# Kernel tuning notes

Hardware: AMD Instinct MI355X
Metric: run time of the kernel (lower is better)

The kernel has to match this reference:

```python
import jax, jax.numpy as jnp
import numpy as np

N = 100000      # nodes
E = 1600000     # edges (avg degree 16)
D = 128         # in_feats
C = 40          # n_classes
K = 4           # propagation steps
T = 2.0
DELTA = T / K   # 0.5
EPS = 1e-5      # LayerNorm eps


def setup_inputs() -> dict:
    key = jax.random.key(0)
    k1, k2, k3, k4, k5 = jax.random.split(key, 5)
    feat = jax.random.normal(k1, (N, D), jnp.float32)
    row = jax.random.randint(k2, (E,), 0, N, dtype=jnp.int32)
    col = jax.random.randint(k3, (E,), 0, N, dtype=jnp.int32)
    # fc: Linear(D -> C), xavier-ish scale
    W = jax.random.normal(k4, (C, D), jnp.float32) / np.sqrt(D)
    b = jax.random.normal(k5, (C,), jnp.float32) * 0.01
    # LayerNorm params
    gamma = jnp.ones((C,), jnp.float32)
    beta = jnp.zeros((C,), jnp.float32)
    return {"feat": feat, "row": row, "col": col, "W": W, "b": b,
            "gamma": gamma, "beta": beta}


def reference(feat, row, col, W, b, gamma, beta):
    # degrees of augmented adjacency A + I (row counts + self loop)
    deg = jnp.zeros((N,), feat.dtype).at[row].add(1.0) + 1.0
    dinv = jax.lax.rsqrt(deg)
    w_edge = dinv[row] * dinv[col]     # S[row,col] for off-diagonal entries
    w_self = dinv * dinv               # S[i,i] from the added self loop
    # h <- ((1-delta) I + delta S)^K @ feat, applied iteratively (same math as
    # precomputing the matrix power, but never materializes it)
    h = feat
    for _ in range(K):
        agg = jax.ops.segment_sum(h[col] * w_edge[:, None], row, num_segments=N)
        agg = agg + h * w_self[:, None]
        h = (1.0 - DELTA) * h + DELTA * agg
    # fc
    h = h @ W.T + b                    # [N, C]
    # LayerNorm over last dim
    mu = jnp.mean(h, axis=-1, keepdims=True)
    var = jnp.var(h, axis=-1, keepdims=True)
    h = (h - mu) * jax.lax.rsqrt(var + EPS) * gamma + beta
    return h
```

## Files before the change

### kernel.cpp

```cpp
#include <hip/hip_runtime.h>
#include <hip/hip_fp16.h>

#define N_NODES 100000
#define N_EDGES 1600000
#define D_FEAT  128
#define C_CLS   40
#define ZSTRIDE 32
#define LN_EPS  1e-5f

#define RPB   256
#define NBKT  ((N_NODES + RPB - 1) / RPB)
#define BCAP  6144
#define TILE_E 4096
#define EBLK  ((N_EDGES + TILE_E - 1) / TILE_E)
#define NTILES (N_NODES / 16)
#define FCB   ((NTILES + 3) / 4)

typedef __attribute__((ext_vector_type(8))) _Float16 half8;
typedef __attribute__((ext_vector_type(4))) float floatx4;
typedef __attribute__((ext_vector_type(2))) int   intx2;
typedef __attribute__((ext_vector_type(4))) unsigned uintx4;

__device__ inline float2 h2f2(unsigned v) {
    __half2 h = *(__half2*)&v;
    return __half22float2(h);
}
__device__ inline unsigned f2h2(float x, float y) {
    __half2 h = __floats2half2_rn(x, y);
    return *(unsigned*)&h;
}

__global__ __launch_bounds__(256) void fcbin_k(const float* __restrict__ feat,
                                               const float* __restrict__ W,
                                               const int* __restrict__ row,
                                               const int* __restrict__ col,
                                               int* __restrict__ bktsz,
                                               int* __restrict__ csr_tmp,
                                               unsigned* __restrict__ z) {
    __shared__ int hist[NBKT];
    __shared__ int cbase[NBKT];
    __shared__ _Float16 zl[4][16][64];
    int t = threadIdx.x;
    if (blockIdx.x < EBLK) {
        int tile = blockIdx.x * TILE_E;
        for (int i = t; i < NBKT; i += 256) hist[i] = 0;
        __syncthreads();
        int r[16], c[16], pos[16];
        #pragma unroll
        for (int k = 0; k < 16; k++) {
            int e = tile + k * 256 + t;
            if (e < N_EDGES) {
                r[k] = row[e]; c[k] = col[e];
                pos[k] = atomicAdd(&hist[r[k] / RPB], 1);
            } else r[k] = -1;
        }
        __syncthreads();
        for (int i = t; i < NBKT; i += 256) {
            int h = hist[i];
            cbase[i] = h ? atomicAdd(&bktsz[i], h) : 0;
        }
        __syncthreads();
        #pragma unroll
        for (int k = 0; k < 16; k++) {
            if (r[k] >= 0) {
                int b = r[k] / RPB;
                int slot = cbase[b] + pos[k];
                if (slot < BCAP)
                    csr_tmp[b * BCAP + slot] = ((r[k] & (RPB - 1)) << 17) | c[k];
            }
        }
        return;
    }
    int wave = t >> 6, lane = t & 63;
    int m = lane & 15, quad = lane >> 4;
    int tile = (blockIdx.x - EBLK) * 4 + wave;
    bool valid = (tile < NTILES);
    int node0 = tile * 16;

    half8 bfrag[3][4];
    if (valid) {
        #pragma unroll
        for (int ct = 0; ct < 3; ct++) {
            int c = ct * 16 + m;
            bool ok = (c < C_CLS);
            #pragma unroll
            for (int ks = 0; ks < 4; ks++) {
                const float* wr = W + c * D_FEAT + ks * 32 + quad * 8;
                #pragma unroll
                for (int j = 0; j < 8; j++)
                    bfrag[ct][ks][j] = ok ? (_Float16)wr[j] : (_Float16)0.0f;
            }
        }
    }

    floatx4 acc0 = {0.f,0.f,0.f,0.f}, acc1 = acc0, acc2 = acc0;
    if (valid) {
        #pragma unroll
        for (int ks = 0; ks < 4; ks++) {
            const float4* ap = (const float4*)&feat[(node0 + m) * D_FEAT + ks * 32 + quad * 8];
            float4 a0 = ap[0], a1 = ap[1];
            half8 afrag;
            afrag[0] = (_Float16)a0.x; afrag[1] = (_Float16)a0.y;
            afrag[2] = (_Float16)a0.z; afrag[3] = (_Float16)a0.w;
            afrag[4] = (_Float16)a1.x; afrag[5] = (_Float16)a1.y;
            afrag[6] = (_Float16)a1.z; afrag[7] = (_Float16)a1.w;
            acc0 = __builtin_amdgcn_mfma_f32_16x16x32_f16(afrag, bfrag[0][ks], acc0, 0, 0, 0);
            acc1 = __builtin_amdgcn_mfma_f32_16x16x32_f16(afrag, bfrag[1][ks], acc1, 0, 0, 0);
            acc2 = __builtin_amdgcn_mfma_f32_16x16x32_f16(afrag, bfrag[2][ks], acc2, 0, 0, 0);
        }
    }

    {
        int zr = lane >> 2;
        uint2 zz = make_uint2(0u, 0u);
        ((uint2*)&zl[wave][zr][48])[lane & 3] = zz;
    }
    if (valid) {
        #pragma unroll
        for (int r = 0; r < 4; r++) {
            int zrow = quad * 4 + r;
            zl[wave][zrow][m]      = (_Float16)acc0[r];
            zl[wave][zrow][16 + m] = (_Float16)acc1[r];
            zl[wave][zrow][32 + m] = (_Float16)acc2[r];
        }
    }
    __syncthreads();
    if (valid) {
        int zr = lane >> 2, part = lane & 3;
        uint4 v0 = ((uint4*)&zl[wave][zr][0])[part];
        uint4 v1 = ((uint4*)&zl[wave][zr][0])[part + 4];
        uint4* zg = (uint4*)z;
        zg[(size_t)(node0 + zr) * 8 + part]     = v0;
        zg[(size_t)(node0 + zr) * 8 + part + 4] = v1;
    }
}

__global__ __launch_bounds__(256) void refineA_k(const int* __restrict__ csr_tmp,
                                                 const int* __restrict__ bktsz,
                                                 int2* __restrict__ rowinfo,
                                                 float* __restrict__ dinv,
                                                 float* __restrict__ selfc) {
    __shared__ int hist[RPB];
    __shared__ int psc[RPB];
    int b = blockIdx.x, t = threadIdx.x;
    int r0 = b * RPB;
    int nrows = min(RPB, N_NODES - r0);
    hist[t] = 0;
    __syncthreads();
    int cnt = bktsz[b];
    const int* base = csr_tmp + b * BCAP;
    for (int i = t; i < cnt; i += 256)
        atomicAdd(&hist[base[i] >> 17], 1);
    __syncthreads();
    int v = hist[t];
    psc[t] = v;
    __syncthreads();
    for (int off = 1; off < 256; off <<= 1) {
        int x = (t >= off) ? psc[t - off] : 0;
        __syncthreads();
        psc[t] += x;
        __syncthreads();
    }
    if (t < nrows) {
        int start = b * BCAP + psc[t] - v;
        float d = rsqrtf((float)v + 1.0f);
        rowinfo[r0 + t] = make_int2(start, start + v);
        dinv[r0 + t]  = d;
        selfc[r0 + t] = 0.5f + 0.5f * d * d;
    }
}

__global__ __launch_bounds__(256) void refineB_k(const int* __restrict__ csr_tmp,
                                                 const int* __restrict__ bktsz,
                                                 const int2* __restrict__ rowinfo,
                                                 const float* __restrict__ dinv,
                                                 int2* __restrict__ csr) {
    __shared__ int   cur[RPB];
    __shared__ float dl[RPB];
    int b = blockIdx.x, t = threadIdx.x;
    int r0 = b * RPB;
    int nrows = min(RPB, N_NODES - r0);
    if (t < nrows) {
        cur[t] = rowinfo[r0 + t].x;
        dl[t]  = dinv[r0 + t];
    }
    __syncthreads();
    int cnt = bktsz[b];
    const int* base = csr_tmp + b * BCAP;
    for (int i = t; i < cnt; i += 256) {
        int pk = base[i];
        int lr = pk >> 17;
        int c  = pk & 0x1FFFF;
        int p = atomicAdd(&cur[lr], 1);
        float w = (0.5f * dl[lr]) * dinv[c];
        csr[p] = make_int2(c, __float_as_int(w));
    }
}

__global__ __launch_bounds__(256) void prop_z_k(const unsigned* __restrict__ hin,
                                                unsigned* __restrict__ hout,
                                                const int2* __restrict__ rowinfo,
                                                const int2* __restrict__ csr,
                                                const float* __restrict__ selfc) {
    int t = threadIdx.x;
    int wave = t >> 6, lane = t & 63;
    int q   = lane >> 3;
    int sub = lane & 7;
    int node = blockIdx.x * 32 + wave * 8 + q;
    const uintx4* hin4 = (const uintx4*)hin;

    uintx4 hv = hin4[(unsigned)node * 8 + sub];
    float sc = selfc[node];
    float acc[8];
    {
        float2 f0 = h2f2(hv.x), f1 = h2f2(hv.y), f2 = h2f2(hv.z), f3 = h2f2(hv.w);
        acc[0] = f0.x * sc; acc[1] = f0.y * sc;
        acc[2] = f1.x * sc; acc[3] = f1.y * sc;
        acc[4] = f2.x * sc; acc[5] = f2.y * sc;
        acc[6] = f3.x * sc; acc[7] = f3.y * sc;
    }

    int2 ri = rowinfo[node];
    int j = ri.x, end = ri.y;
    int base = ri.x;

    int2 e[8];
    #pragma unroll
    for (int k = 0; k < 8; k++) {
        int idx = (j + k < end) ? j + k : base;
        e[k] = csr[idx];
    }

    while (__any(j < end)) {
        uintx4 g[8];
        float w[8];
        #pragma unroll
        for (int k = 0; k < 8; k++) {
            bool val = (j + k < end);
            int  c   = val ? e[k].x : 0;
            w[k]     = val ? __int_as_float(e[k].y) : 0.0f;
            g[k] = hin4[(unsigned)c * 8 + sub];
        }
        int j2 = j + 8;
        #pragma unroll
        for (int k = 0; k < 8; k++) {
            int idx = (j2 + k < end) ? j2 + k : base;
            e[k] = csr[idx];
        }
        #pragma unroll
        for (int k = 0; k < 8; k++) {
            float2 f0 = h2f2(g[k].x), f1 = h2f2(g[k].y), f2 = h2f2(g[k].z), f3 = h2f2(g[k].w);
            acc[0] += w[k] * f0.x; acc[1] += w[k] * f0.y;
            acc[2] += w[k] * f1.x; acc[3] += w[k] * f1.y;
            acc[4] += w[k] * f2.x; acc[5] += w[k] * f2.y;
            acc[6] += w[k] * f3.x; acc[7] += w[k] * f3.y;
        }
        j = j2;
    }

    uintx4 o;
    o.x = f2h2(acc[0], acc[1]);
    o.y = f2h2(acc[2], acc[3]);
    o.z = f2h2(acc[4], acc[5]);
    o.w = f2h2(acc[6], acc[7]);
    ((uintx4*)hout)[(unsigned)node * 8 + sub] = o;
}

__global__ __launch_bounds__(256) void ln_k(const unsigned* __restrict__ z,
                                            const float* __restrict__ b,
                                            const float* __restrict__ gamma,
                                            const float* __restrict__ beta,
                                            float* __restrict__ out) {
    int t = threadIdx.x;
    int node = blockIdx.x * 64 + (t >> 2);
    int p = t & 2 ? (t & 3) : (t & 3);
    p = t & 3;
    if (node >= N_NODES) return;

    float v[16];
    float s = 0.0f, ss = 0.0f;
    int cb = p * 16;
    int nreal = (p < 2) ? 16 : (p == 2 ? 8 : 0);
    if (nreal) {
        const uint4* zr = (const uint4*)z + (size_t)node * 8;
        uint4 a0 = zr[p * 2], a1 = zr[p * 2 + 1];
        unsigned u[8] = {a0.x, a0.y, a0.z, a0.w, a1.x, a1.y, a1.z, a1.w};
        #pragma unroll
        for (int i = 0; i < 8; i++) {
            float2 f = h2f2(u[i]);
            v[2 * i] = f.x; v[2 * i + 1] = f.y;
        }
        for (int i = 0; i < nreal; i++) {
            v[i] += b[cb + i];
            s += v[i];
            ss += v[i] * v[i];
        }
    }
    s  += __shfl_xor(s, 1);  s  += __shfl_xor(s, 2);
    ss += __shfl_xor(ss, 1); ss += __shfl_xor(ss, 2);

    float mean = s * (1.0f / C_CLS);
    float var  = ss * (1.0f / C_CLS) - mean * mean;
    float inv  = rsqrtf(var + LN_EPS);
    if (nreal) {
        float* orow = out + (size_t)node * C_CLS + cb;
        for (int i = 0; i < nreal; i++)
            orow[i] = (v[i] - mean) * inv * gamma[cb + i] + beta[cb + i];
    }
}

extern "C" void kernel_launch(void* const* d_in, const int* in_sizes, int n_in,
                              void* d_out, int out_size, void* d_ws, size_t ws_size,
                              hipStream_t stream) {
    const float* feat  = (const float*)d_in[0];
    const int*   row   = (const int*)d_in[1];
    const int*   col   = (const int*)d_in[2];
    const float* W     = (const float*)d_in[3];
    const float* b     = (const float*)d_in[4];
    const float* gamma = (const float*)d_in[5];
    const float* beta  = (const float*)d_in[6];
    float* out = (float*)d_out;

    char* ws = (char*)d_ws;
    size_t off = 0;
    auto alloc = [&](size_t bytes) {
        size_t o = off;
        off = (off + bytes + 255) & ~(size_t)255;
        return o;
    };
    float*    dinv     = (float*)   (ws + alloc((size_t)N_NODES * 4));
    float*    selfc    = (float*)   (ws + alloc((size_t)N_NODES * 4));
    int2*     rowinfo  = (int2*)    (ws + alloc((size_t)N_NODES * 8));
    int*      bktsz    = (int*)     (ws + alloc((size_t)NBKT * 4));
    int*      csr_tmp  = (int*)     (ws + alloc((size_t)NBKT * BCAP * 4));
    int2*     csr      = (int2*)    (ws + alloc((size_t)NBKT * BCAP * 8));
    unsigned* z0       = (unsigned*)(ws + alloc((size_t)N_NODES * ZSTRIDE * 4));
    unsigned* z1       = (unsigned*)(ws + alloc((size_t)N_NODES * ZSTRIDE * 4));

    (void)hipMemsetAsync(bktsz, 0, (size_t)NBKT * 4, stream);

    fcbin_k<<<EBLK + FCB, 256, 0, stream>>>(feat, W, row, col, bktsz, csr_tmp, z0);
    refineA_k<<<NBKT, 256, 0, stream>>>(csr_tmp, bktsz, rowinfo, dinv, selfc);
    refineB_k<<<NBKT, 256, 0, stream>>>(csr_tmp, bktsz, rowinfo, dinv, csr);

    int pgrid = N_NODES / 32;
    prop_z_k<<<pgrid, 256, 0, stream>>>(z0, z1, rowinfo, csr, selfc);
    prop_z_k<<<pgrid, 256, 0, stream>>>(z1, z0, rowinfo, csr, selfc);
    prop_z_k<<<pgrid, 256, 0, stream>>>(z0, z1, rowinfo, csr, selfc);
    prop_z_k<<<pgrid, 256, 0, stream>>>(z1, z0, rowinfo, csr, selfc);

    int lblocks = (N_NODES + 63) / 64;
    ln_k<<<lblocks, 256, 0, stream>>>(z0, b, gamma, beta, out);
}
```

Baseline: 331.0 us.

## Fuse LayerNorm into last propagation step and compute degrees via global atomics

The final propagation step now applies the bias, LayerNorm and the output write directly from its registers, which removes the separate ln_k kernel and one round trip of the fp16 intermediate through memory. Per-row degrees are now counted with global atomics in extra blocks of the binning kernel. That lets the old refine step, which re-read the bucketed edges to build a histogram, become a simple prefix scan over the degree array. The shared tile row is also padded from 64 to 72 halves, likely to cut LDS bank conflicts. The trade-offs are more global atomic traffic on row indices, an extra memset, and idle lanes in the fused LayerNorm tail.

Result: slower. 365.9 us (+10.6%).

```diff
diff --git a/kernel.cpp b/kernel.cpp
--- a/kernel.cpp
+++ b/kernel.cpp
@@ -15,10 +15,10 @@
 #define EBLK  ((N_EDGES + TILE_E - 1) / TILE_E)
 #define NTILES (N_NODES / 16)
 #define FCB   ((NTILES + 3) / 4)
+#define DEGB  ((N_EDGES + 256*8 - 1) / (256*8))
 
 typedef __attribute__((ext_vector_type(8))) _Float16 half8;
 typedef __attribute__((ext_vector_type(4))) float floatx4;
-typedef __attribute__((ext_vector_type(2))) int   intx2;
 typedef __attribute__((ext_vector_type(4))) unsigned uintx4;
 
 __device__ inline float2 h2f2(unsigned v) {
@@ -35,12 +35,22 @@
                                                const int* __restrict__ row,
                                                const int* __restrict__ col,
                                                int* __restrict__ bktsz,
+                                               int* __restrict__ deg,
                                                int* __restrict__ csr_tmp,
                                                unsigned* __restrict__ z) {
+    int t = threadIdx.x;
+    if (blockIdx.x >= EBLK + FCB) {
+        int e0 = (blockIdx.x - (EBLK + FCB)) * (256 * 8) + t;
+        #pragma unroll
+        for (int k = 0; k < 8; k++) {
+            int e = e0 + k * 256;
+            if (e < N_EDGES) atomicAdd(&deg[row[e]], 1);
+        }
+        return;
+    }
     __shared__ int hist[NBKT];
     __shared__ int cbase[NBKT];
-    __shared__ _Float16 zl[4][16][64];
-    int t = threadIdx.x;
+    __shared__ _Float16 zl[4][16][72];
     if (blockIdx.x < EBLK) {
         int tile = blockIdx.x * TILE_E;
         for (int i = t; i < NBKT; i += 256) hist[i] = 0;
@@ -135,24 +145,14 @@
     }
 }
 
-__global__ __launch_bounds__(256) void refineA_k(const int* __restrict__ csr_tmp,
-                                                 const int* __restrict__ bktsz,
+__global__ __launch_bounds__(256) void rowscan_k(const int* __restrict__ deg,
                                                  int2* __restrict__ rowinfo,
                                                  float* __restrict__ dinv,
                                                  float* __restrict__ selfc) {
-    __shared__ int hist[RPB];
     __shared__ int psc[RPB];
     int b = blockIdx.x, t = threadIdx.x;
-    int r0 = b * RPB;
-    int nrows = min(RPB, N_NODES - r0);
-    hist[t] = 0;
-    __syncthreads();
-    int cnt = bktsz[b];
-    const int* base = csr_tmp + b * BCAP;
-    for (int i = t; i < cnt; i += 256)
-        atomicAdd(&hist[base[i] >> 17], 1);
-    __syncthreads();
-    int v = hist[t];
+    int r = b * RPB + t;
+    int v = (r < N_NODES) ? deg[r] : 0;
     psc[t] = v;
     __syncthreads();
     for (int off = 1; off < 256; off <<= 1) {
@@ -161,12 +161,12 @@
         psc[t] += x;
         __syncthreads();
     }
-    if (t < nrows) {
+    if (r < N_NODES) {
         int start = b * BCAP + psc[t] - v;
         float d = rsqrtf((float)v + 1.0f);
-        rowinfo[r0 + t] = make_int2(start, start + v);
-        dinv[r0 + t]  = d;
-        selfc[r0 + t] = 0.5f + 0.5f * d * d;
+        rowinfo[r] = make_int2(start, start + v);
+        dinv[r]    = d;
+        selfc[r]   = 0.5f + 0.5f * d * d;
     }
 }
 
@@ -197,11 +197,16 @@
     }
 }
 
-__global__ __launch_bounds__(256) void prop_z_k(const unsigned* __restrict__ hin,
+template<bool FINAL>
+__global__ __launch_bounds__(256) void prop_z_t(const unsigned* __restrict__ hin,
                                                 unsigned* __restrict__ hout,
                                                 const int2* __restrict__ rowinfo,
                                                 const int2* __restrict__ csr,
-                                                const float* __restrict__ selfc) {
+                                                const float* __restrict__ selfc,
+                                                const float* __restrict__ bias,
+                                                const float* __restrict__ gamma,
+                                                const float* __restrict__ beta,
+                                                float* __restrict__ out) {
     int t = threadIdx.x;
     int wave = t >> 6, lane = t & 63;
     int q   = lane >> 3;
@@ -258,54 +263,38 @@
         j = j2;
     }
 
-    uintx4 o;
-    o.x = f2h2(acc[0], acc[1]);
-    o.y = f2h2(acc[2], acc[3]);
-    o.z = f2h2(acc[4], acc[5]);
-    o.w = f2h2(acc[6], acc[7]);
-    ((uintx4*)hout)[(unsigned)node * 8 + sub] = o;
-}
-
-__global__ __launch_bounds__(256) void ln_k(const unsigned* __restrict__ z,
-                                            const float* __restrict__ b,
-                                            const float* __restrict__ gamma,
-                                            const float* __restrict__ beta,
-                                            float* __restrict__ out) {
-    int t = threadIdx.x;
-    int node = blockIdx.x * 64 + (t >> 2);
-    int p = t & 2 ? (t & 3) : (t & 3);
-    p = t & 3;
-    if (node >= N_NODES) return;
-
-    float v[16];
-    float s = 0.0f, ss = 0.0f;
-    int cb = p * 16;
-    int nreal = (p < 2) ? 16 : (p == 2 ? 8 : 0);
-    if (nreal) {
-        const uint4* zr = (const uint4*)z + (size_t)node * 8;
-        uint4 a0 = zr[p * 2], a1 = zr[p * 2 + 1];
-        unsigned u[8] = {a0.x, a0.y, a0.z, a0.w, a1.x, a1.y, a1.z, a1.w};
+    if (!FINAL) {
+        uintx4 o;
+        o.x = f2h2(acc[0], acc[1]);
+        o.y = f2h2(acc[2], acc[3]);
+        o.z = f2h2(acc[4], acc[5]);
+        o.w = f2h2(acc[6], acc[7]);
+        ((uintx4*)hout)[(unsigned)node * 8 + sub] = o;
+    } else {
+        bool realsub = (sub < 5);
+        int cb = sub * 8;
+        float v[8];
+        float s = 0.0f, ss = 0.0f;
         #pragma unroll
         for (int i = 0; i < 8; i++) {
-            float2 f = h2f2(u[i]);
-            v[2 * i] = f.x; v[2 * i + 1] = f.y;
-        }
-        for (int i = 0; i < nreal; i++) {
-            v[i] += b[cb + i];
-            s += v[i];
-            ss += v[i] * v[i];
-        }
-    }
-    s  += __shfl_xor(s, 1);  s  += __shfl_xor(s, 2);
-    ss += __shfl_xor(ss, 1); ss += __shfl_xor(ss, 2);
-
-    float mean = s * (1.0f / C_CLS);
-    float var  = ss * (1.0f / C_CLS) - mean * mean;
-    float inv  = rsqrtf(var + LN_EPS);
-    if (nreal) {
-        float* orow = out + (size_t)node * C_CLS + cb;
-        for (int i = 0; i < nreal; i++)
-            orow[i] = (v[i] - mean) * inv * gamma[cb + i] + beta[cb + i];
+            float vv = realsub ? (acc[i] + bias[cb + i]) : 0.0f;
+            v[i] = vv;
+            s += vv; ss += vv * vv;
+        }
+        s  += __shfl_xor(s, 1);  s  += __shfl_xor(s, 2);  s  += __shfl_xor(s, 4);
+        ss += __shfl_xor(ss, 1); ss += __shfl_xor(ss, 2); ss += __shfl_xor(ss, 4);
+        float mean = s * (1.0f / C_CLS);
+        float var  = ss * (1.0f / C_CLS) - mean * mean;
+        float inv  = rsqrtf(var + LN_EPS);
+        if (realsub) {
+            float o8[8];
+            #pragma unroll
+            for (int i = 0; i < 8; i++)
+                o8[i] = (v[i] - mean) * inv * gamma[cb + i] + beta[cb + i];
+            float* orow = out + (size_t)node * C_CLS + cb;
+            ((float4*)orow)[0] = make_float4(o8[0], o8[1], o8[2], o8[3]);
+            ((float4*)orow)[1] = make_float4(o8[4], o8[5], o8[6], o8[7]);
+        }
     }
 }
 
@@ -332,23 +321,26 @@
     float*    selfc    = (float*)   (ws + alloc((size_t)N_NODES * 4));
     int2*     rowinfo  = (int2*)    (ws + alloc((size_t)N_NODES * 8));
     int*      bktsz    = (int*)     (ws + alloc((size_t)NBKT * 4));
+    int*      deg      = (int*)     (ws + alloc((size_t)N_NODES * 4));
     int*      csr_tmp  = (int*)     (ws + alloc((size_t)NBKT * BCAP * 4));
     int2*     csr      = (int2*)    (ws + alloc((size_t)NBKT * BCAP * 8));
     unsigned* z0       = (unsigned*)(ws + alloc((size_t)N_NODES * ZSTRIDE * 4));
     unsigned* z1       = (unsigned*)(ws + alloc((size_t)N_NODES * ZSTRIDE * 4));
 
     (void)hipMemsetAsync(bktsz, 0, (size_t)NBKT * 4, stream);
-
-    fcbin_k<<<EBLK + FCB, 256, 0, stream>>>(feat, W, row, col, bktsz, csr_tmp, z0);
-    refineA_k<<<NBKT, 256, 0, stream>>>(csr_tmp, bktsz, rowinfo, dinv, selfc);
+    (void)hipMemsetAsync(deg, 0, (size_t)N_NODES * 4, stream);
+
+    fcbin_k<<<EBLK + FCB + DEGB, 256, 0, stream>>>(feat, W, row, col, bktsz, deg, csr_tmp, z0);
+    rowscan_k<<<NBKT, 256, 0, stream>>>(deg, rowinfo, dinv, selfc);
     refineB_k<<<NBKT, 256, 0, stream>>>(csr_tmp, bktsz, rowinfo, dinv, csr);
 
     int pgrid = N_NODES / 32;
-    prop_z_k<<<pgrid, 256, 0, stream>>>(z0, z1, rowinfo, csr, selfc);
-    prop_z_k<<<pgrid, 256, 0, stream>>>(z1, z0, rowinfo, csr, selfc);
-    prop_z_k<<<pgrid, 256, 0, stream>>>(z0, z1, rowinfo, csr, selfc);
-    prop_z_k<<<pgrid, 256, 0, stream>>>(z1, z0, rowinfo, csr, selfc);
-
-    int lblocks = (N_NODES + 63) / 64;
-    ln_k<<<lblocks, 256, 0, stream>>>(z0, b, gamma, beta, out);
-}
+    prop_z_t<false><<<pgrid, 256, 0, stream>>>(z0, z1, rowinfo, csr, selfc,
+                                               nullptr, nullptr, nullptr, nullptr);
+    prop_z_t<false><<<pgrid, 256, 0, stream>>>(z1, z0, rowinfo, csr, selfc,
+                                               nullptr, nullptr, nullptr, nullptr);
+    prop_z_t<false><<<pgrid, 256, 0, stream>>>(z0, z1, rowinfo, csr, selfc,
+                                               nullptr, nullptr, nullptr, nullptr);
+    prop_z_t<true><<<pgrid, 256, 0, stream>>>(z1, nullptr, rowinfo, csr, selfc,
+                                              b, gamma, beta, out);
+}
```
